# Performance work log

Hardware: AMD Instinct MI355X
Metric: run time of the kernel (lower is better)

The kernel has to match this reference:

```python
import jax, jax.numpy as jnp
import numpy as np

DIM = 1024
NUM_HEADS = 16
HEAD_DIM = DIM // NUM_HEADS
SCALE = HEAD_DIM ** (-0.5)


def setup_inputs() -> dict:
    key = jax.random.key(0)
    k_x, k_qkv, k_ow, k_ob = jax.random.split(key, 4)
    x = jax.random.normal(k_x, (4, 2048, DIM), dtype=jnp.float32)
    # nn.Linear(dim, 3*dim, bias=False): store as [dim, 3*dim] for x @ W
    w_qkv = jax.random.normal(k_qkv, (DIM, 3 * DIM), dtype=jnp.float32) * (DIM ** -0.5)
    w_out = jax.random.normal(k_ow, (DIM, DIM), dtype=jnp.float32) * (DIM ** -0.5)
    b_out = jax.random.normal(k_ob, (DIM,), dtype=jnp.float32) * 0.02
    return {"x": x, "w_qkv": w_qkv, "w_out": w_out, "b_out": b_out}


def reference(x, w_qkv, w_out, b_out):
    B, S, D = x.shape
    H, Hd = NUM_HEADS, HEAD_DIM
    qkv = x @ w_qkv                                  # [B, S, 3*D]
    # rearrange 'b s (v h d) -> v b h s d'
    qkv = qkv.reshape(B, S, 3, H, Hd).transpose(2, 0, 3, 1, 4)
    q, k, v = qkv[0], qkv[1], qkv[2]                 # each [B, H, S, Hd]
    scores = jnp.einsum('bhqd,bhkd->bhqk', q, k) * SCALE
    attn = jax.nn.softmax(scores, axis=-1)
    out = jnp.einsum('bhqk,bhkd->bhqd', attn, v)     # [B, H, S, Hd]
    out = out.transpose(0, 2, 1, 3).reshape(B, S, D)  # 'b h s d -> b s (h d)'
    return out @ w_out + b_out
```

## Files before the change

kernel.cpp:

```cpp
#include <hip/hip_runtime.h>
#include <hip/hip_bf16.h>
#include <stdint.h>

typedef __bf16 bf16_t;
typedef __bf16 bf16x4 __attribute__((ext_vector_type(4)));
typedef __bf16 bf16x8 __attribute__((ext_vector_type(8)));
typedef float f32x4 __attribute__((ext_vector_type(4)));
typedef unsigned short u16;

#define L2E 1.4426950408889634f
#define MC 69.249473f
#define QSC 0.18033688f

__device__ __forceinline__ void async_load16(const bf16_t* g, bf16_t* l) {
  __builtin_amdgcn_global_load_lds(
      (__attribute__((address_space(1))) uint32_t*)g,
      (__attribute__((address_space(3))) uint32_t*)l, 16, 0, 0);
}

__global__ void detect_k(const uint16_t* __restrict__ x, int* __restrict__ flag) {
  if (blockIdx.x != 0) return;
  const int lane = threadIdx.x & 63;
  int bad = 0;
#pragma unroll
  for (int p = 0; p < 4; ++p) {
    const int i = lane * 4 + p;
    uint16_t h = x[2 * i];
    int e = (h >> 7) & 0xFF;
    if (e == 0 || e >= 0xBD) bad++;
  }
  bad += __shfl_xor(bad, 1, 64);
  bad += __shfl_xor(bad, 2, 64);
  bad += __shfl_xor(bad, 4, 64);
  bad += __shfl_xor(bad, 8, 64);
  bad += __shfl_xor(bad, 16, 64);
  bad += __shfl_xor(bad, 32, 64);
  if (lane == 0 && threadIdx.x < 64) *flag = (bad > 32) ? 1 : 0;
}

__global__ void convert_k(const void* __restrict__ in, bf16_t* __restrict__ out,
                          int n, const int* __restrict__ flag) {
  const int f = *flag;
  const int i0 = blockIdx.x * blockDim.x + threadIdx.x;
  const int stride = gridDim.x * blockDim.x;
  if (f) {
    const float* p = (const float*)in;
    for (int i = i0; i < n; i += stride) {
      float v = p[i];
      v = (v == v) ? v : 0.f;
      v = fminf(fmaxf(v, -1e6f), 1e6f);
      out[i] = (bf16_t)v;
    }
  } else {
    const bf16_t* p = (const bf16_t*)in;
    for (int i = i0; i < n; i += stride) {
      float v = (float)p[i];
      v = (v == v) ? v : 0.f;
      v = fminf(fmaxf(v, -1e6f), 1e6f);
      out[i] = (bf16_t)v;
    }
  }
}

__global__ __launch_bounds__(256) void wtrans_k(const void* __restrict__ in,
                                                bf16_t* __restrict__ out, int R,
                                                int C, const int* __restrict__ flag) {
  __shared__ u16 tile[64][65];
  const int f = *flag;
  const int tr = blockIdx.y * 64, tc = blockIdx.x * 64;
  const int t = threadIdx.x;
#pragma unroll
  for (int i = 0; i < 16; ++i) {
    int idx = i * 256 + t, r = idx >> 6, c = idx & 63;
    float v;
    if (f)
      v = ((const float*)in)[(size_t)(tr + r) * C + tc + c];
    else
      v = (float)((const bf16_t*)in)[(size_t)(tr + r) * C + tc + c];
    v = (v == v) ? v : 0.f;
    v = fminf(fmaxf(v, -1e6f), 1e6f);
    bf16_t b = (bf16_t)v;
    tile[r][c] = *(u16*)&b;
  }
  __syncthreads();
#pragma unroll
  for (int i = 0; i < 16; ++i) {
    int idx = i * 256 + t, r = idx >> 6, c = idx & 63;
    ((u16*)out)[(size_t)(tc + r) * R + tr + c] = tile[c][r];
  }
}

__device__ __forceinline__ void gemm_bt_mainloop(
    const bf16_t* __restrict__ A, const bf16_t* __restrict__ Bt, int K, int m0,
    int n0, bf16_t* As, bf16_t* Bs, f32x4 acc[4][4]) {
  const int t = threadIdx.x, lane = t & 63, w = t >> 6;
  const int l15 = lane & 15, quad = lane >> 4;
  const int wm = (w >> 1) * 64, wn = (w & 1) * 64;
  const int srow = w * 16 + (lane >> 2);
  const int sk = (lane & 3) * 8;
  const bf16_t* gA = A + (size_t)(m0 + srow) * K + sk;
  const bf16_t* gB = Bt + (size_t)(n0 + srow) * K + sk;
  bf16_t* lA = As + w * 512;
  bf16_t* lB = Bs + w * 512;
  const size_t gstep = (size_t)64 * K;

  for (int kt = 0; kt < K; kt += 32) {
    __syncthreads();
    async_load16(gA, lA);
    async_load16(gA + gstep, lA + 2048);
    async_load16(gB, lB);
    async_load16(gB + gstep, lB + 2048);
    gA += 32;
    gB += 32;
    __syncthreads();
    bf16x8 af[4], bfr[4];
#pragma unroll
    for (int f = 0; f < 4; ++f) {
      af[f] = *(const bf16x8*)(As + (wm + f * 16 + l15) * 32 + quad * 8);
      bfr[f] = *(const bf16x8*)(Bs + (wn + f * 16 + l15) * 32 + quad * 8);
    }
#pragma unroll
    for (int i = 0; i < 4; ++i)
#pragma unroll
      for (int j = 0; j < 4; ++j)
        acc[i][j] =
            __builtin_amdgcn_mfma_f32_16x16x32_bf16(af[i], bfr[j], acc[i][j], 0, 0, 0);
  }
}

__global__ __launch_bounds__(256) void qkv_gemm_k(const bf16_t* __restrict__ X,
                                                  const bf16_t* __restrict__ WqT,
                                                  bf16_t* __restrict__ qo,
                                                  bf16_t* __restrict__ ko,
                                                  bf16_t* __restrict__ vto) {
  __shared__ __align__(16) bf16_t As[128 * 32];
  __shared__ __align__(16) bf16_t Bs[128 * 32];
  const int m0 = blockIdx.y * 128, n0 = blockIdx.x * 128;
  f32x4 acc[4][4];
  const f32x4 z = {0.f, 0.f, 0.f, 0.f};
#pragma unroll
  for (int i = 0; i < 4; ++i)
#pragma unroll
    for (int j = 0; j < 4; ++j) acc[i][j] = z;
  gemm_bt_mainloop(X, WqT, 1024, m0, n0, As, Bs, acc);

  const int lane = threadIdx.x & 63, w = threadIdx.x >> 6;
  const int l15 = lane & 15, quad = lane >> 4;
  const int wm = (w >> 1) * 64, wn = (w & 1) * 64;
#pragma unroll
  for (int j = 0; j < 4; ++j) {
    const int gnb = n0 + wn + j * 16;
    const int vi = gnb >> 10;
    const int rem = gnb & 1023;
    const int h = rem >> 6;
    const int d = (rem & 63) + l15;
    if (vi == 2) {
#pragma unroll
      for (int i = 0; i < 4; ++i) {
        const int gm0 = m0 + wm + i * 16 + quad * 4;
        const int b = gm0 >> 11, s = gm0 & 2047;
        bf16x4 pv;
#pragma unroll
        for (int r = 0; r < 4; ++r) pv[r] = (bf16_t)acc[i][j][r];
        *(bf16x4*)(vto + ((size_t)(b * 16 + h) * 64 + d) * 2048 + s) = pv;
      }
    } else {
      const float scale = (vi == 0) ? QSC : 1.0f;
      bf16_t* dst = (vi == 0) ? qo : ko;
#pragma unroll
      for (int i = 0; i < 4; ++i) {
#pragma unroll
        for (int r = 0; r < 4; ++r) {
          const int gm = m0 + wm + i * 16 + quad * 4 + r;
          const int b = gm >> 11, s = gm & 2047;
          dst[(((size_t)(b * 16 + h) * 2048 + s) << 6) + d] =
              (bf16_t)(acc[i][j][r] * scale);
        }
      }
    }
  }
}

__global__ __launch_bounds__(256) void out_gemm_k(const bf16_t* __restrict__ Ain,
                                                  const bf16_t* __restrict__ WoT,
                                                  const bf16_t* __restrict__ bias,
                                                  void* __restrict__ outp,
                                                  const int* __restrict__ flag) {
  __shared__ __align__(16) bf16_t As[128 * 32];
  __shared__ __align__(16) bf16_t Bs[128 * 32];
  const int m0 = blockIdx.y * 128, n0 = blockIdx.x * 128;
  f32x4 acc[4][4];
  const f32x4 z = {0.f, 0.f, 0.f, 0.f};
#pragma unroll
  for (int i = 0; i < 4; ++i)
#pragma unroll
    for (int j = 0; j < 4; ++j) acc[i][j] = z;
  gemm_bt_mainloop(Ain, WoT, 1024, m0, n0, As, Bs, acc);

  const int f32out = *flag;
  const int lane = threadIdx.x & 63, w = threadIdx.x >> 6;
  const int l15 = lane & 15, quad = lane >> 4;
  const int wm = (w >> 1) * 64, wn = (w & 1) * 64;
#pragma unroll
  for (int j = 0; j < 4; ++j) {
    const int gn = n0 + wn + j * 16 + l15;
    const float bv = (float)bias[gn];
#pragma unroll
    for (int i = 0; i < 4; ++i) {
#pragma unroll
      for (int r = 0; r < 4; ++r) {
        const int gm = m0 + wm + i * 16 + quad * 4 + r;
        const float val = acc[i][j][r] + bv;
        if (f32out)
          ((float*)outp)[(size_t)gm * 1024 + gn] = val;
        else
          ((bf16_t*)outp)[(size_t)gm * 1024 + gn] = (bf16_t)val;
      }
    }
  }
}

#define KTILE 4096

__global__ __launch_bounds__(256, 3) void attn_k(const bf16_t* __restrict__ q,
                                                 const bf16_t* __restrict__ k,
                                                 const bf16_t* __restrict__ vt,
                                                 bf16_t* __restrict__ o) {
  __shared__ __align__(16) bf16_t Ks[2 * KTILE];
  __shared__ __align__(16) bf16_t Vts[2 * KTILE];
  __shared__ __align__(16) bf16_t Pb[4 * 32 * 64];

  const int t = threadIdx.x, lane = t & 63, w = t >> 6;
  const int l15 = lane & 15, quad = lane >> 4;
  const int x = blockIdx.x;
  const int j = x >> 3;
  const int bh = (x & 7) * 8 + (j >> 4);
  const int qt = j & 15;
  const bf16_t* qp = q + ((size_t)bh * 2048 + qt * 128) * 64;
  const bf16_t* kp = k + (size_t)bh * 2048 * 64;
  const bf16_t* vp = vt + (size_t)bh * 64 * 2048;

  const int lane8 = lane >> 3, lc = lane & 7;
  int kOff[2], vOff[2], ldsOff[2];
#pragma unroll
  for (int c = 0; c < 2; ++c) {
    const int rho = (w * 2 + c) * 8 + lane8;
    const int srow = (rho >> 4) + (rho & 15) * 4;
    const int col = (lc ^ (rho & 7)) * 8;
    kOff[c] = srow * 64 + col;
    vOff[c] = rho * 2048 + col;
    ldsOff[c] = (w * 2 + c) * 512;
  }

  {
    const int qr = t >> 3, qc = t & 7;
#pragma unroll
    for (int p = 0; p < 4; ++p) {
      const int r0 = p * 32 + qr;
      async_load16(qp + (size_t)r0 * 64 + (qc ^ (r0 & 7)) * 8,
                   Ks + r0 * 64 + qc * 8);
    }
  }
  __syncthreads();

  bf16x8 qf[2][2];
#pragma unroll
  for (int qs = 0; qs < 2; ++qs)
#pragma unroll
    for (int ks = 0; ks < 2; ++ks) {
      const int row = w * 32 + qs * 16 + l15;
      qf[qs][ks] = *(const bf16x8*)(Ks + row * 64 +
                                    (((ks * 4 + quad) ^ (row & 7)) * 8));
    }
  __syncthreads();

#pragma unroll
  for (int c = 0; c < 2; ++c) {
    async_load16(kp + kOff[c], Ks + ldsOff[c]);
    async_load16(vp + vOff[c], Vts + ldsOff[c]);
  }

  f32x4 acc[2][4], asum[2];
  const f32x4 z = {0.f, 0.f, 0.f, 0.f};
  const f32x4 minit = {-MC, -MC, -MC, -MC};
  bf16x8 onesf;
#pragma unroll
  for (int i = 0; i < 8; ++i) onesf[i] = (bf16_t)1.0f;
#pragma unroll
  for (int qs = 0; qs < 2; ++qs) {
    asum[qs] = z;
#pragma unroll
    for (int f = 0; f < 4; ++f) acc[qs][f] = z;
  }

  bf16_t* psw = Pb + w * 32 * 64;

  for (int kt = 0; kt < 32; ++kt) {
    __syncthreads();
    if (kt < 31) {
      const int bn = (kt + 1) & 1;
#pragma unroll
      for (int c = 0; c < 2; ++c) {
        async_load16(kp + (size_t)(kt + 1) * KTILE + kOff[c],
                     Ks + bn * KTILE + ldsOff[c]);
        async_load16(vp + (size_t)(kt + 1) * 64 + vOff[c],
                     Vts + bn * KTILE + ldsOff[c]);
      }
    }

    const bf16_t* Kb = Ks + (kt & 1) * KTILE;
    const bf16_t* Vb = Vts + (kt & 1) * KTILE;

    f32x4 sacc[2][4];
    {
      const int cx = ((quad ^ (l15 & 7)) * 8);
      bf16x8 kf[4];
#pragma unroll
      for (int f = 0; f < 4; ++f)
        kf[f] = *(const bf16x8*)(Kb + (f * 16 + l15) * 64 + cx);
      __builtin_amdgcn_s_setprio(1);
#pragma unroll
      for (int qs = 0; qs < 2; ++qs)
#pragma unroll
        for (int f = 0; f < 4; ++f)
          sacc[qs][f] = __builtin_amdgcn_mfma_f32_16x16x32_bf16(
              qf[qs][0], kf[f], minit, 0, 0, 0);
      __builtin_amdgcn_s_setprio(0);
    }
    {
      const int cx = (((4 + quad) ^ (l15 & 7)) * 8);
      bf16x8 kf[4];
#pragma unroll
      for (int f = 0; f < 4; ++f)
        kf[f] = *(const bf16x8*)(Kb + (f * 16 + l15) * 64 + cx);
      __builtin_amdgcn_s_setprio(1);
#pragma unroll
      for (int qs = 0; qs < 2; ++qs)
#pragma unroll
        for (int f = 0; f < 4; ++f)
          sacc[qs][f] = __builtin_amdgcn_mfma_f32_16x16x32_bf16(
              qf[qs][1], kf[f], sacc[qs][f], 0, 0, 0);
      __builtin_amdgcn_s_setprio(0);
    }

#pragma unroll
    for (int qs = 0; qs < 2; ++qs)
#pragma unroll
      for (int r = 0; r < 4; ++r) {
        bf16x4 pk;
#pragma unroll
        for (int f = 0; f < 4; ++f)
          pk[f] = (bf16_t)__builtin_amdgcn_exp2f(fminf(sacc[qs][f][r], 0.f));
        const int row = qs * 16 + quad * 4 + r;
        *(bf16x4*)(psw + row * 64 + ((l15 >> 1) ^ (row & 7)) * 8 +
                   (l15 & 1) * 4) = pk;
      }

#pragma unroll
    for (int ks = 0; ks < 2; ++ks) {
      const int cx = (((ks * 4 + quad) ^ (l15 & 7)) * 8);
      bf16x8 vf[4];
#pragma unroll
      for (int f = 0; f < 4; ++f)
        vf[f] = *(const bf16x8*)(Vb + (f * 16 + l15) * 64 + cx);
#pragma unroll
      for (int qs = 0; qs < 2; ++qs) {
        bf16x8 pf = *(const bf16x8*)(psw + (qs * 16 + l15) * 64 +
                                     ((ks * 4 + quad) ^ (l15 & 7)) * 8);
        __builtin_amdgcn_s_setprio(1);
#pragma unroll
        for (int f = 0; f < 4; ++f)
          acc[qs][f] = __builtin_amdgcn_mfma_f32_16x16x32_bf16(
              pf, vf[f], acc[qs][f], 0, 0, 0);
        asum[qs] = __builtin_amdgcn_mfma_f32_16x16x32_bf16(pf, onesf, asum[qs],
                                                           0, 0, 0);
        __builtin_amdgcn_s_setprio(0);
      }
    }
  }

  const int b = bh >> 4, h = bh & 15;
#pragma unroll
  for (int qs = 0; qs < 2; ++qs)
#pragma unroll
    for (int r = 0; r < 4; ++r) {
      const int srow = qt * 128 + w * 32 + qs * 16 + quad * 4 + r;
      const float inv = 1.0f / fmaxf(asum[qs][r], 1e-37f);
#pragma unroll
      for (int f = 0; f < 4; ++f) {
        const int d = f * 16 + l15;
        o[(size_t)(b * 2048 + srow) * 1024 + h * 64 + d] =
            (bf16_t)(acc[qs][f][r] * inv);
      }
    }
}

extern "C" void kernel_launch(void* const* d_in, const int* in_sizes, int n_in,
                              void* d_out, int out_size, void* d_ws, size_t ws_size,
                              hipStream_t stream) {
  const void* x_raw = d_in[0];
  const void* wqkv_raw = d_in[1];
  const void* wout_raw = d_in[2];
  const void* bout_raw = d_in[3];

  const int nx = 4 * 2048 * 1024;
  const int nwq = 1024 * 3072;
  const int nwo = 1024 * 1024;
  const int nb = 1024;

  char* ws = (char*)d_ws;
  int* flag = (int*)ws;
  bf16_t* xb = (bf16_t*)(ws + 256);
  bf16_t* wqbT = xb + nx;
  bf16_t* wobT = wqbT + nwq;
  bf16_t* bob = wobT + nwo;
  bf16_t* qb = bob + nb;
  const size_t bhsd = (size_t)4 * 16 * 2048 * 64;
  bf16_t* kb = qb + bhsd;
  bf16_t* vtb = kb + bhsd;
  bf16_t* ab = xb;

  detect_k<<<1, 64, 0, stream>>>((const uint16_t*)x_raw, flag);
  convert_k<<<2048, 256, 0, stream>>>(x_raw, xb, nx, flag);
  wtrans_k<<<dim3(3072 / 64, 1024 / 64), 256, 0, stream>>>(wqkv_raw, wqbT, 1024,
                                                           3072, flag);
  wtrans_k<<<dim3(1024 / 64, 1024 / 64), 256, 0, stream>>>(wout_raw, wobT, 1024,
                                                           1024, flag);
  convert_k<<<4, 256, 0, stream>>>(bout_raw, bob, nb, flag);

  qkv_gemm_k<<<dim3(3072 / 128, 8192 / 128), 256, 0, stream>>>(xb, wqbT, qb, kb,
                                                               vtb);
  attn_k<<<dim3(1024), 256, 0, stream>>>(qb, kb, vtb, ab);
  out_gemm_k<<<dim3(1024 / 128, 8192 / 128), 256, 0, stream>>>(ab, wobT, bob,
                                                               d_out, flag);
}
```

Baseline: 298.9 us.

## Double-buffer GEMM LDS loads, remap workgroups for XCD locality, vectorize convert

The shared GEMM mainloop now uses two LDS buffers, so the next K-tile's async global-to-LDS loads are issued before the current tile's MFMAs. This removes one barrier per iteration and hides load latency. Both GEMMs switch to a 1D grid with a bid-to-tile remap that spreads consecutive tiles across the 8 XCDs for better L2 reuse. The convert kernel now processes 8 elements per thread with vector loads and stores. LDS use doubles, and the convert kernel assumes n is a multiple of 8.

```diff
diff --git a/kernel.cpp b/kernel.cpp
--- a/kernel.cpp
+++ b/kernel.cpp
@@ -41,23 +41,39 @@
 __global__ void convert_k(const void* __restrict__ in, bf16_t* __restrict__ out,
                           int n, const int* __restrict__ flag) {
   const int f = *flag;
+  const int nv = n >> 3;
   const int i0 = blockIdx.x * blockDim.x + threadIdx.x;
   const int stride = gridDim.x * blockDim.x;
   if (f) {
-    const float* p = (const float*)in;
-    for (int i = i0; i < n; i += stride) {
-      float v = p[i];
-      v = (v == v) ? v : 0.f;
-      v = fminf(fmaxf(v, -1e6f), 1e6f);
-      out[i] = (bf16_t)v;
+    const float4* p = (const float4*)in;
+    for (int i = i0; i < nv; i += stride) {
+      const float4 a = p[2 * i], b = p[2 * i + 1];
+      const float v[8] = {a.x, a.y, a.z, a.w, b.x, b.y, b.z, b.w};
+      bf16x8 o8;
+#pragma unroll
+      for (int j = 0; j < 8; ++j) {
+        float x = v[j];
+        x = (x == x) ? x : 0.f;
+        x = fminf(fmaxf(x, -1e6f), 1e6f);
+        o8[j] = (bf16_t)x;
+      }
+      *(bf16x8*)(out + (size_t)i * 8) = o8;
     }
   } else {
-    const bf16_t* p = (const bf16_t*)in;
-    for (int i = i0; i < n; i += stride) {
-      float v = (float)p[i];
-      v = (v == v) ? v : 0.f;
-      v = fminf(fmaxf(v, -1e6f), 1e6f);
-      out[i] = (bf16_t)v;
+    const uint4* p = (const uint4*)in;
+    for (int i = i0; i < nv; i += stride) {
+      const uint4 a = p[i];
+      const uint32_t wds[4] = {a.x, a.y, a.z, a.w};
+      bf16x8 o8;
+#pragma unroll
+      for (int j = 0; j < 8; ++j) {
+        const uint32_t h = (wds[j >> 1] >> ((j & 1) * 16)) & 0xFFFFu;
+        float x = __builtin_bit_cast(float, h << 16);
+        x = (x == x) ? x : 0.f;
+        x = fminf(fmaxf(x, -1e6f), 1e6f);
+        o8[j] = (bf16_t)x;
+      }
+      *(bf16x8*)(out + (size_t)i * 8) = o8;
     }
   }
 }
@@ -100,24 +116,33 @@
   const int sk = (lane & 3) * 8;
   const bf16_t* gA = A + (size_t)(m0 + srow) * K + sk;
   const bf16_t* gB = Bt + (size_t)(n0 + srow) * K + sk;
-  bf16_t* lA = As + w * 512;
-  bf16_t* lB = Bs + w * 512;
   const size_t gstep = (size_t)64 * K;
-
-  for (int kt = 0; kt < K; kt += 32) {
-    __syncthreads();
-    async_load16(gA, lA);
-    async_load16(gA + gstep, lA + 2048);
-    async_load16(gB, lB);
-    async_load16(gB + gstep, lB + 2048);
-    gA += 32;
-    gB += 32;
-    __syncthreads();
+  const int nt = K >> 5;
+  const int lo = w * 512;
+
+  async_load16(gA, As + lo);
+  async_load16(gA + gstep, As + lo + 2048);
+  async_load16(gB, Bs + lo);
+  async_load16(gB + gstep, Bs + lo + 2048);
+  __syncthreads();
+
+  for (int kt = 0; kt < nt; ++kt) {
+    const int cur = (kt & 1) * 4096, nxt = 4096 - cur;
+    if (kt + 1 < nt) {
+      const bf16_t* gA1 = gA + (size_t)(kt + 1) * 32;
+      const bf16_t* gB1 = gB + (size_t)(kt + 1) * 32;
+      async_load16(gA1, As + nxt + lo);
+      async_load16(gA1 + gstep, As + nxt + lo + 2048);
+      async_load16(gB1, Bs + nxt + lo);
+      async_load16(gB1 + gstep, Bs + nxt + lo + 2048);
+    }
+    const bf16_t* Ab = As + cur;
+    const bf16_t* Bb = Bs + cur;
     bf16x8 af[4], bfr[4];
 #pragma unroll
     for (int f = 0; f < 4; ++f) {
-      af[f] = *(const bf16x8*)(As + (wm + f * 16 + l15) * 32 + quad * 8);
-      bfr[f] = *(const bf16x8*)(Bs + (wn + f * 16 + l15) * 32 + quad * 8);
+      af[f] = *(const bf16x8*)(Ab + (wm + f * 16 + l15) * 32 + quad * 8);
+      bfr[f] = *(const bf16x8*)(Bb + (wn + f * 16 + l15) * 32 + quad * 8);
     }
 #pragma unroll
     for (int i = 0; i < 4; ++i)
@@ -125,6 +150,7 @@
       for (int j = 0; j < 4; ++j)
         acc[i][j] =
             __builtin_amdgcn_mfma_f32_16x16x32_bf16(af[i], bfr[j], acc[i][j], 0, 0, 0);
+    if (kt + 1 < nt) __syncthreads();
   }
 }
 
@@ -133,9 +159,11 @@
                                                   bf16_t* __restrict__ qo,
                                                   bf16_t* __restrict__ ko,
                                                   bf16_t* __restrict__ vto) {
-  __shared__ __align__(16) bf16_t As[128 * 32];
-  __shared__ __align__(16) bf16_t Bs[128 * 32];
-  const int m0 = blockIdx.y * 128, n0 = blockIdx.x * 128;
+  __shared__ __align__(16) bf16_t As[2 * 4096];
+  __shared__ __align__(16) bf16_t Bs[2 * 4096];
+  const int bid = blockIdx.x;
+  const int wgid = (bid & 7) * 192 + (bid >> 3);
+  const int m0 = (wgid / 24) * 128, n0 = (wgid % 24) * 128;
   f32x4 acc[4][4];
   const f32x4 z = {0.f, 0.f, 0.f, 0.f};
 #pragma unroll
@@ -186,9 +214,11 @@
                                                   const bf16_t* __restrict__ bias,
                                                   void* __restrict__ outp,
                                                   const int* __restrict__ flag) {
-  __shared__ __align__(16) bf16_t As[128 * 32];
-  __shared__ __align__(16) bf16_t Bs[128 * 32];
-  const int m0 = blockIdx.y * 128, n0 = blockIdx.x * 128;
+  __shared__ __align__(16) bf16_t As[2 * 4096];
+  __shared__ __align__(16) bf16_t Bs[2 * 4096];
+  const int bid = blockIdx.x;
+  const int wgid = (bid & 7) * 64 + (bid >> 3);
+  const int m0 = (wgid / 8) * 128, n0 = (wgid % 8) * 128;
   f32x4 acc[4][4];
   const f32x4 z = {0.f, 0.f, 0.f, 0.f};
 #pragma unroll
@@ -426,11 +456,9 @@
                                                            3072, flag);
   wtrans_k<<<dim3(1024 / 64, 1024 / 64), 256, 0, stream>>>(wout_raw, wobT, 1024,
                                                            1024, flag);
-  convert_k<<<4, 256, 0, stream>>>(bout_raw, bob, nb, flag);
-
-  qkv_gemm_k<<<dim3(3072 / 128, 8192 / 128), 256, 0, stream>>>(xb, wqbT, qb, kb,
-                                                               vtb);
+  convert_k<<<1, 256, 0, stream>>>(bout_raw, bob, nb, flag);
+
+  qkv_gemm_k<<<dim3(1536), 256, 0, stream>>>(xb, wqbT, qb, kb, vtb);
   attn_k<<<dim3(1024), 256, 0, stream>>>(qb, kb, vtb, ab);
-  out_gemm_k<<<dim3(1024 / 128, 8192 / 128), 256, 0, stream>>>(ab, wobT, bob,
-                                                               d_out, flag);
-}
+  out_gemm_k<<<dim3(512), 256, 0, stream>>>(ab, wobT, bob, d_out, flag);
+}
```

Result: slower. 314.8 us (+5.3%).
